# Performance work log

Measured on AMD Instinct MI355X. Metric: run time of the kernel, lower is better.

The kernel has to match this reference:

```python
import jax, jax.numpy as jnp
import numpy as np

# blocks, d_model, heads, ffn_hidden, vocab, gen_len=(image_size//4)**2
L, D, NH, FF, V, GEN = 4, 256, 8, 1024, 2048, 16
B, NS, SLOT = 8, 7, 256  # batch, num_slots+1 (slots + projected action), slot_size


def setup_inputs():
    key = jax.random.key(0)
    ks = jax.random.split(key, 16)
    def n(i, shape, s=0.02):
        return (jax.random.normal(ks[i], shape) * s).astype(jnp.float32)
    return dict(
        slots=jax.random.normal(ks[0], (B, NS, SLOT), dtype=jnp.float32),
        W_slot_proj=n(1, (SLOT, D)),
        dict_emb=n(2, (V + 1, D)),
        pe=n(3, (GEN + 1, D)),
        ln_self_w=jnp.ones((L, D)), ln_self_b=jnp.zeros((L, D)),
        Wq_s=n(4, (L, D, D)), Wk_s=n(5, (L, D, D)), Wv_s=n(6, (L, D, D)), Wo_s=n(7, (L, D, D)),
        ln_cross_w=jnp.ones((L, D)), ln_cross_b=jnp.zeros((L, D)),
        Wq_c=n(8, (L, D, D)), Wk_c=n(9, (L, D, D)), Wv_c=n(10, (L, D, D)), Wo_c=n(11, (L, D, D)),
        ln_ffn_w=jnp.ones((L, D)), ln_ffn_b=jnp.zeros((L, D)),
        W1=n(12, (L, D, FF)), b1=jnp.zeros((L, FF)),
        W2=n(13, (L, FF, D)), b2=jnp.zeros((L, D)),
        ln_f_w=jnp.ones((D,)), ln_f_b=jnp.zeros((D,)),
        W_out=n(14, (D, V)),
    )


def _ln(x, w, b, eps=1e-5):
    m = x.mean(-1, keepdims=True)
    v = ((x - m) ** 2).mean(-1, keepdims=True)
    return (x - m) * jax.lax.rsqrt(v + eps) * w + b


def _mha(q_in, k_in, v_in, Wq, Wk, Wv, Wo, mask=None):
    Bq, Tq, Dm = q_in.shape
    dh = Dm // NH
    q = (q_in @ Wq).reshape(Bq, Tq, NH, dh).transpose(0, 2, 1, 3) * (dh ** -0.5)
    k = (k_in @ Wk).reshape(Bq, -1, NH, dh).transpose(0, 2, 1, 3)
    v = (v_in @ Wv).reshape(Bq, -1, NH, dh).transpose(0, 2, 1, 3)
    att = jnp.einsum('bhqd,bhkd->bhqk', q, k)
    if mask is not None:
        att = att + mask
    att = jax.nn.softmax(att, axis=-1)
    o = jnp.einsum('bhqk,bhkd->bhqd', att, v)
    return o.transpose(0, 2, 1, 3).reshape(Bq, Tq, Dm) @ Wo


def _decoder(x, enc, P):
    T = x.shape[1]
    i = jnp.arange(T)
    mask = jnp.where(i[:, None] >= i[None, :], 0.0, -jnp.inf).astype(x.dtype)
    for l in range(L):
        h = _ln(x, P['ln_self_w'][l], P['ln_self_b'][l])
        if l == 0:
            x = h  # SLATE: first block normalizes residual stream in-place
        x = x + _mha(h, h, h, P['Wq_s'][l], P['Wk_s'][l], P['Wv_s'][l], P['Wo_s'][l], mask)
        h = _ln(x, P['ln_cross_w'][l], P['ln_cross_b'][l])
        x = x + _mha(h, enc, enc, P['Wq_c'][l], P['Wk_c'][l], P['Wv_c'][l], P['Wo_c'][l])
        h = _ln(x, P['ln_ffn_w'][l], P['ln_ffn_b'][l])
        x = x + (jax.nn.relu(h @ P['W1'][l] + P['b1'][l]) @ P['W2'][l] + P['b2'][l])
    return _ln(x, P['ln_f_w'], P['ln_f_b'])


def _slots2tokens(slots, W_slot_proj, dict_emb, pe, P, W_out):
    Bb = slots.shape[0]
    enc = slots @ W_slot_proj  # slot_proj (bias=False)
    Tf = GEN + 1
    # fixed-size token buffer; position 0 is BOS one-hot, future slots are zeros
    # (causal mask guarantees they never influence position t's output)
    buf = jnp.zeros((Bb, Tf, V + 1), jnp.float32).at[:, 0, 0].set(1.0)

    def step(buf, t):
        tok = jnp.argmax(buf, axis=-1)              # [B, Tf]
        emb = dict_emb[tok] + pe[None, :Tf]         # OneHotDictionary + PositionalEncoding
        dec = _decoder(emb, enc, P)
        logits_t = dec[:, t] @ W_out                # [B, V]
        z_next = jax.nn.one_hot(jnp.argmax(logits_t, -1), V, dtype=buf.dtype)
        upd = jnp.pad(z_next, ((0, 0), (1, 0)))[:, None, :]  # prepend BOS column
        buf = jax.lax.dynamic_update_slice(buf, upd, (0, t + 1, 0))
        return buf, (z_next, logits_t)

    _, (z_gen, logits) = jax.lax.scan(step, buf, jnp.arange(GEN))
    z_gen = jnp.moveaxis(z_gen, 0, 1)    # [B, GEN, V]
    logits = jnp.moveaxis(logits, 0, 1)  # [B, GEN, V]
    He = int(np.sqrt(GEN))               # H_enc = W_enc = image_size // 4
    z_img = z_gen.transpose(0, 2, 1).reshape(Bb, V, He, He)
    return z_img, jax.nn.log_softmax(logits, axis=-1)


def reference(slots, W_slot_proj, dict_emb, pe, ln_self_w, ln_self_b, Wq_s, Wk_s, Wv_s, Wo_s, ln_cross_w, ln_cross_b, Wq_c, Wk_c, Wv_c, Wo_c, ln_ffn_w, ln_ffn_b, W1, b1, W2, b2, ln_f_w, ln_f_b, W_out):
    P = dict(ln_self_w=ln_self_w, ln_self_b=ln_self_b, Wq_s=Wq_s, Wk_s=Wk_s, Wv_s=Wv_s, Wo_s=Wo_s,
             ln_cross_w=ln_cross_w, ln_cross_b=ln_cross_b, Wq_c=Wq_c, Wk_c=Wk_c, Wv_c=Wv_c, Wo_c=Wo_c,
             ln_ffn_w=ln_ffn_w, ln_ffn_b=ln_ffn_b, W1=W1, b1=b1, W2=W2, b2=b2,
             ln_f_w=ln_f_w, ln_f_b=ln_f_b)
    return _slots2tokens(slots, W_slot_proj, dict_emb, pe, P, W_out)
```

## Files before the change

### kernel.cpp

```cpp
#include <hip/hip_runtime.h>

#define D       256
#define DH      32
#define FFDIM   1024
#define VOCAB   2048
#define GENLEN  16
#define BATCH   8
#define NSLOT   7
#define TF      17
#define NLAYER  4

#define SCOPE_AGENT __HIP_MEMORY_SCOPE_AGENT

typedef float    f32x4 __attribute__((ext_vector_type(4)));
typedef unsigned u32x4 __attribute__((ext_vector_type(4)));
typedef unsigned long long u64;

struct Params {
  const float *slots, *W_slot_proj, *dict_emb, *pe;
  const float *ln_self_w, *ln_self_b, *Wq_s, *Wk_s, *Wv_s, *Wo_s;
  const float *ln_cross_w, *ln_cross_b, *Wq_c, *Wk_c, *Wv_c, *Wo_c;
  const float *ln_ffn_w, *ln_ffn_b, *W1, *b1, *W2, *b2;
  const float *ln_f_w, *ln_f_b, *W_out;
  float *enc;
  u64 *P0, *P1, *tri;
  unsigned *flags;
  float *out_z, *out_lp;
};

__device__ __forceinline__ float cload(const float* p) {
  return __hip_atomic_load(p, __ATOMIC_RELAXED, SCOPE_AGENT);
}
__device__ __forceinline__ void cstore(float* p, float v) {
  __hip_atomic_store(p, v, __ATOMIC_RELAXED, SCOPE_AGENT);
}
__device__ __forceinline__ u64 cload64(const u64* p) {
  return __hip_atomic_load(p, __ATOMIC_RELAXED, SCOPE_AGENT);
}
__device__ __forceinline__ void cstore64(u64* p, u64 v) {
  __hip_atomic_store(p, v, __ATOMIC_RELAXED, SCOPE_AGENT);
}
__device__ __forceinline__ u64 packt(unsigned tag, float v) {
  return ((u64)tag << 32) | (u64)__float_as_uint(v);
}

__device__ __forceinline__ float blockSum(float v, float* red) {
  #pragma unroll
  for (int o = 32; o > 0; o >>= 1) v += __shfl_down(v, o);
  const int lane = threadIdx.x & 63, w = threadIdx.x >> 6;
  if (lane == 0) red[w] = v;
  __syncthreads();
  float s = red[0] + red[1] + red[2] + red[3];
  __syncthreads();
  return s;
}

template<int N>
__device__ __forceinline__ float dotStreamPre(const float* __restrict__ W,
                                              const float* __restrict__ h,
                                              int i0, int ld,
                                              const float* __restrict__ pre) {
  float pA[32], pB[32];
  #pragma unroll
  for (int k = 0; k < 32; ++k) pA[k] = pre[k];
  #pragma unroll
  for (int k = 0; k < 32; ++k) pB[k] = W[(size_t)(i0 + 32 + k) * ld];
  float acc = 0.f;
  #pragma unroll 1
  for (int u = 0; u < N; u += 64) {
    const f32x4* h4 = reinterpret_cast<const f32x4*>(h + i0 + u);
    #pragma unroll
    for (int k = 0; k < 8; ++k) {
      const f32x4 hv = h4[k];
      acc = fmaf(hv.x, pA[4*k+0], acc); acc = fmaf(hv.y, pA[4*k+1], acc);
      acc = fmaf(hv.z, pA[4*k+2], acc); acc = fmaf(hv.w, pA[4*k+3], acc);
    }
    if (u + 64 < N) {
      #pragma unroll
      for (int k = 0; k < 32; ++k) pA[k] = W[(size_t)(i0 + u + 64 + k) * ld];
    }
    #pragma unroll
    for (int k = 0; k < 8; ++k) {
      const f32x4 hv = h4[8 + k];
      acc = fmaf(hv.x, pB[4*k+0], acc); acc = fmaf(hv.y, pB[4*k+1], acc);
      acc = fmaf(hv.z, pB[4*k+2], acc); acc = fmaf(hv.w, pB[4*k+3], acc);
    }
    if (u + 96 < N) {
      #pragma unroll
      for (int k = 0; k < 32; ++k) pB[k] = W[(size_t)(i0 + u + 96 + k) * ld];
    }
  }
  return acc;
}

template<int N>
__device__ __forceinline__ float dotStream(const float* __restrict__ W,
                                           const float* __restrict__ h,
                                           int i0, int ld) {
  float pre[32];
  #pragma unroll
  for (int k = 0; k < 32; ++k) pre[k] = W[(size_t)(i0 + k) * ld];
  return dotStreamPre<N>(W, h, i0, ld, pre);
}

__device__ __forceinline__ float dot32(const float* __restrict__ w,
                                       const float* __restrict__ h, int i0) {
  float acc = 0.f;
  const f32x4* h4 = reinterpret_cast<const f32x4*>(h + i0);
  #pragma unroll
  for (int k = 0; k < 8; ++k) {
    const f32x4 hv = h4[k];
    acc = fmaf(hv.x, w[4*k+0], acc); acc = fmaf(hv.y, w[4*k+1], acc);
    acc = fmaf(hv.z, w[4*k+2], acc); acc = fmaf(hv.w, w[4*k+3], acc);
  }
  return acc;
}

__global__ __launch_bounds__(256, 1) void mega_kernel(Params p)
{
  const int blk = blockIdx.x;
  const int bb = blk >> 3, sl = blk & 7, tid = threadIdx.x;
  unsigned* flags = p.flags + bb * 256;

  __shared__ __align__(16) float hsh[D];
  __shared__ __align__(16) float ash[128];
  __shared__ float qsh[DH], osh[DH], score[TF], red[4];
  __shared__ float wval[4]; __shared__ int widx[4];
  __shared__ float stage[NSLOT * D];
  __shared__ float kls[NLAYER][TF][DH + 1], vls[NLAYER][TF][DH + 1];
  __shared__ float kcls[NLAYER][NSLOT][DH + 1], vcls[NLAYER][NSLOT][DH + 1];

  auto fold8t = [&](const u64* P, unsigned exp) -> float {
    const u64* a0 = P + (bb * 8 + 0) * 256 + tid;
    const u64* a2 = P + (bb * 8 + 2) * 256 + tid;
    const u64* a4 = P + (bb * 8 + 4) * 256 + tid;
    const u64* a6 = P + (bb * 8 + 6) * 256 + tid;
    u64 v0, v1, v2, v3, v4, v5, v6, v7;
    for (;;) {
      asm volatile(
        "global_load_dwordx2 %0, %8, off sc0 sc1\n\t"
        "global_load_dwordx2 %1, %8, off offset:2048 sc0 sc1\n\t"
        "global_load_dwordx2 %2, %9, off sc0 sc1\n\t"
        "global_load_dwordx2 %3, %9, off offset:2048 sc0 sc1\n\t"
        "global_load_dwordx2 %4, %10, off sc0 sc1\n\t"
        "global_load_dwordx2 %5, %10, off offset:2048 sc0 sc1\n\t"
        "global_load_dwordx2 %6, %11, off sc0 sc1\n\t"
        "global_load_dwordx2 %7, %11, off offset:2048 sc0 sc1\n\t"
        "s_waitcnt vmcnt(0)"
        : "=&v"(v0), "=&v"(v1), "=&v"(v2), "=&v"(v3),
          "=&v"(v4), "=&v"(v5), "=&v"(v6), "=&v"(v7)
        : "v"(a0), "v"(a2), "v"(a4), "v"(a6) : "memory");
      if ((unsigned)(v0 >> 32) == exp && (unsigned)(v1 >> 32) == exp &&
          (unsigned)(v2 >> 32) == exp && (unsigned)(v3 >> 32) == exp &&
          (unsigned)(v4 >> 32) == exp && (unsigned)(v5 >> 32) == exp &&
          (unsigned)(v6 >> 32) == exp && (unsigned)(v7 >> 32) == exp)
        break;
      __builtin_amdgcn_s_sleep(1);
    }
    const float s0 = __uint_as_float((unsigned)v0), s1 = __uint_as_float((unsigned)v1);
    const float s2 = __uint_as_float((unsigned)v2), s3 = __uint_as_float((unsigned)v3);
    const float s4 = __uint_as_float((unsigned)v4), s5 = __uint_as_float((unsigned)v5);
    const float s6 = __uint_as_float((unsigned)v6), s7 = __uint_as_float((unsigned)v7);
    return ((s0 + s1) + (s2 + s3)) + ((s4 + s5) + (s6 + s7));
  };

  float heldLogit = 0.f;
  int   lastAmax  = 0;

  auto consume_tri = [&](int row, unsigned exp) {
    float smax8[8], ssum8[8]; int sarg8[8];
    for (;;) {
      bool ok = true;
      #pragma unroll
      for (int j = 0; j < 8; ++j) {
        const u64 A = cload64(&p.tri[(bb * 8 + j) * 4 + 0]);
        const u64 B = cload64(&p.tri[(bb * 8 + j) * 4 + 1]);
        const u64 C = cload64(&p.tri[(bb * 8 + j) * 4 + 2]);
        ok = ok && ((unsigned)(A >> 32) == exp) && ((unsigned)(B >> 32) == exp)
                && ((unsigned)(C >> 32) == exp);
        smax8[j] = __uint_as_float((unsigned)A);
        ssum8[j] = __uint_as_float((unsigned)B);
        sarg8[j] = (int)(unsigned)C;
      }
      if (ok) break;
      __builtin_amdgcn_s_sleep(1);
    }
    float gm = smax8[0];
    #pragma unroll
    for (int j = 1; j < 8; ++j) gm = fmaxf(gm, smax8[j]);
    float gs = 0.f; float best = -1e30f; int am = 0;
    #pragma unroll
    for (int j = 0; j < 8; ++j) {
      gs += ssum8[j] * expf(smax8[j] - gm);
      if (smax8[j] > best) { best = smax8[j]; am = j * 256 + sarg8[j]; }
    }
    const float lse = gm + logf(gs);
    p.out_lp[(bb * GENLEN + row) * VOCAB + sl * 256 + tid] = heldLogit - lse;
    if (sl == 0 && tid == 0)
      p.out_z[bb * VOCAB * GENLEN + am * GENLEN + row] = 1.0f;
    lastAmax = am;
  };

  for (int i = tid; i < NLAYER * TF * (DH + 1); i += 256) {
    (&kls[0][0][0])[i] = 0.f;
    (&vls[0][0][0])[i] = 0.f;
  }

  if (tid < 32) {
    const int c = sl * 32 + tid;
    float acc[NSLOT] = {0.f,0.f,0.f,0.f,0.f,0.f,0.f};
    #pragma unroll 8
    for (int i = 0; i < D; ++i) {
      const float w = p.W_slot_proj[i * D + c];
      #pragma unroll
      for (int s = 0; s < NSLOT; ++s) acc[s] += p.slots[(bb * NSLOT + s) * D + i] * w;
    }
    for (int s = 0; s < NSLOT; ++s) cstore(&p.enc[(bb * NSLOT + s) * D + c], acc[s]);
  }
  {
    __syncthreads();
    if (tid == 0) __hip_atomic_store(flags + sl, 1u, __ATOMIC_RELAXED, SCOPE_AGENT);
    if (tid == 0) {
      u32x4 f0, f1;
      for (;;) {
        asm volatile(
          "global_load_dwordx4 %0, %2, off sc0 sc1\n\t"
          "global_load_dwordx4 %1, %2, off offset:16 sc0 sc1\n\t"
          "s_waitcnt vmcnt(0)"
          : "=&v"(f0), "=&v"(f1) : "v"(flags) : "memory");
        if (f0.x >= 1u && f0.y >= 1u && f0.z >= 1u && f0.w >= 1u &&
            f1.x >= 1u && f1.y >= 1u && f1.z >= 1u && f1.w >= 1u)
          break;
        __builtin_amdgcn_s_sleep(1);
      }
    }
    __syncthreads();
    asm volatile("" ::: "memory");
  }

  {
    for (int i = tid; i < NSLOT * D; i += 256) stage[i] = cload(&p.enc[bb * NSLOT * D + i]);
    __syncthreads();
    const int l = tid >> 6, g = tid & 63, c32 = g >> 1, mat = g & 1;
    const float* W = (mat ? p.Wv_c : p.Wk_c) + l * D * D + sl * DH + c32;
    float acc[NSLOT] = {0.f,0.f,0.f,0.f,0.f,0.f,0.f};
    #pragma unroll 8
    for (int i = 0; i < D; ++i) {
      const float w = W[i * D];
      #pragma unroll
      for (int s = 0; s < NSLOT; ++s) acc[s] += stage[s * D + i] * w;
    }
    if (mat) { for (int s = 0; s < NSLOT; ++s) vcls[l][s][c32] = acc[s]; }
    else     { for (int s = 0; s < NSLOT; ++s) kcls[l][s][c32] = acc[s]; }
    __syncthreads();
  }

  u64* Pbuf[2] = {p.P0, p.P1};
  int par = 0;
  unsigned ctr = 0;
  float x = 0.f;

  #pragma unroll 1
  for (int t = 0; t < GENLEN; ++t) {
    #pragma unroll 1
    for (int l = 0; l < NLAYER; ++l) {
      {
        const unsigned expect = ctr; ++ctr; const unsigned wtag = ctr;
        const int mm = tid >> 6, g = tid & 63, c32 = g >> 1, half = g & 1;
        const float* Wqkv = (mm == 0 ? p.Wq_s : (mm == 1 ? p.Wk_s : p.Wv_s))
                          + l * D * D + sl * DH + c32;
        float preq[32];
        if (tid < 192) {
          #pragma unroll
          for (int k = 0; k < 32; ++k) preq[k] = Wqkv[(size_t)(half * 128 + k) * D];
        }
        float wo[32];
        {
          const float* W = p.Wo_s + l * D * D + sl * DH * D + tid;
          #pragma unroll
          for (int k = 0; k < 32; ++k) wo[k] = W[(size_t)k * D];
        }

        if (l == 0) {
          int tok = 0;
          if (t > 0) { consume_tri(t - 1, expect); tok = lastAmax + 1; }
          x = p.dict_emb[tok * D + tid] + p.pe[t * D + tid];
        } else {
          x += fold8t(Pbuf[par], expect);
        }
        const float h = blockSum(x, red) * 0.f + x;
        const float mean = blockSum(x, red) * (1.f / D);
        const float dv = x - mean;
        const float var = blockSum(dv * dv, red) * (1.f / D);
        const float hval = dv * (1.f / sqrtf(var + 1e-5f)) * p.ln_self_w[l * D + tid]
                         + p.ln_self_b[l * D + tid];
        (void)h;
        if (l == 0) x = hval;
        hsh[tid] = hval;
        __syncthreads();

        if (tid < 192) {
          float acc = dotStreamPre<128>(Wqkv, hsh, half * 128, D, preq);
          acc += __shfl_xor(acc, 1);
          if (half == 0) {
            if (mm == 0)      qsh[c32] = acc * 0.17677669529663689f;
            else if (mm == 1) kls[l][t][c32] = acc;
            else              vls[l][t][c32] = acc;
          }
        }
        __syncthreads();

        if (tid < 64) {
          float s = -1e30f;
          if (tid <= t) {
            float a = 0.f;
            #pragma unroll
            for (int r = 0; r < DH; ++r) a += qsh[r] * kls[l][tid][r];
            s = a;
          }
          float m = s;
          #pragma unroll
          for (int o = 32; o > 0; o >>= 1) m = fmaxf(m, __shfl_xor(m, o));
          const float e = (tid <= t) ? expf(s - m) : 0.f;
          float sum = e;
          #pragma unroll
          for (int o = 32; o > 0; o >>= 1) sum += __shfl_xor(sum, o);
          const float inv = 1.f / sum;
          if (tid < TF) score[tid] = e * inv;
        }
        __syncthreads();
        if (tid < DH) {
          float a = 0.f;
          #pragma unroll
          for (int pp = 0; pp < TF; ++pp) a = fmaf(score[pp], vls[l][pp][tid], a);
          osh[tid] = a;
        }
        __syncthreads();
        {
          float a0 = 0.f;
          #pragma unroll
          for (int k = 0; k < 32; ++k) a0 = fmaf(osh[k], wo[k], a0);
          cstore64(&Pbuf[par ^ 1][(bb * 8 + sl) * 256 + tid], packt(wtag, a0));
        }
        par ^= 1;
      }

      {
        const unsigned expect = ctr; ++ctr; const unsigned wtag = ctr;
        const int c32 = tid >> 3, sub = tid & 7;
        float wq[32], woc[32];
        {
          const float* W = p.Wq_c + l * D * D + sl * DH + c32;
          #pragma unroll
          for (int k = 0; k < 32; ++k) wq[k] = W[(size_t)(sub * 32 + k) * D];
        }
        {
          const float* W = p.Wo_c + l * D * D + sl * DH * D + tid;
          #pragma unroll
          for (int k = 0; k < 32; ++k) woc[k] = W[(size_t)k * D];
        }

        x += fold8t(Pbuf[par], expect);
        const float mean = blockSum(x, red) * (1.f / D);
        const float dv = x - mean;
        const float var = blockSum(dv * dv, red) * (1.f / D);
        hsh[tid] = dv * (1.f / sqrtf(var + 1e-5f)) * p.ln_cross_w[l * D + tid]
                 + p.ln_cross_b[l * D + tid];
        __syncthreads();

        {
          float acc = dot32(wq, hsh, sub * 32);
          acc += __shfl_xor(acc, 1);
          acc += __shfl_xor(acc, 2);
          acc += __shfl_xor(acc, 4);
          if (sub == 0) qsh[c32] = acc * 0.17677669529663689f;
        }
        __syncthreads();

        if (tid < 64) {
          float s = -1e30f;
          if (tid < NSLOT) {
            float a = 0.f;
            #pragma unroll
            for (int r = 0; r < DH; ++r) a += qsh[r] * kcls[l][tid][r];
            s = a;
          }
          float m = s;
          #pragma unroll
          for (int o = 32; o > 0; o >>= 1) m = fmaxf(m, __shfl_xor(m, o));
          const float e = (tid < NSLOT) ? expf(s - m) : 0.f;
          float sum = e;
          #pragma unroll
          for (int o = 32; o > 0; o >>= 1) sum += __shfl_xor(sum, o);
          const float inv = 1.f / sum;
          if (tid < NSLOT) score[tid] = e * inv;
        }
        __syncthreads();
        if (tid < DH) {
          float a = 0.f;
          #pragma unroll
          for (int s = 0; s < NSLOT; ++s) a = fmaf(score[s], vcls[l][s][tid], a);
          osh[tid] = a;
        }
        __syncthreads();
        {
          float a0 = 0.f;
          #pragma unroll
          for (int k = 0; k < 32; ++k) a0 = fmaf(osh[k], woc[k], a0);
          cstore64(&Pbuf[par ^ 1][(bb * 8 + sl) * 256 + tid], packt(wtag, a0));
        }
        par ^= 1;
      }

      {
        const unsigned expect = ctr; ++ctr; const unsigned wtag = ctr;
        const int c128 = tid >> 1, half = tid & 1, c = sl * 128 + c128;
        const float* W1p = p.W1 + l * D * FFDIM + c;
        float prew1[32];
        {
          #pragma unroll
          for (int k = 0; k < 32; ++k) prew1[k] = W1p[(size_t)(half * 128 + k) * FFDIM];
        }

        x += fold8t(Pbuf[par], expect);
        const float mean = blockSum(x, red) * (1.f / D);
        const float dv = x - mean;
        const float var = blockSum(dv * dv, red) * (1.f / D);
        hsh[tid] = dv * (1.f / sqrtf(var + 1e-5f)) * p.ln_ffn_w[l * D + tid]
                 + p.ln_ffn_b[l * D + tid];
        __syncthreads();

        {
          float acc = dotStreamPre<128>(W1p, hsh, half * 128, FFDIM, prew1);
          acc += __shfl_xor(acc, 1);
          if (half == 0) ash[c128] = fmaxf(acc + p.b1[l * FFDIM + c], 0.f);
        }
        __syncthreads();
        {
          float acc = dotStream<128>(p.W2 + l * FFDIM * D + sl * 128 * D + tid, ash, 0, D);
          if (sl == 0) acc += p.b2[l * D + tid];
          cstore64(&Pbuf[par ^ 1][(bb * 8 + sl) * 256 + tid], packt(wtag, acc));
        }
        __syncthreads();
      }
      par ^= 1;
    }

    {
      const unsigned expect = ctr; ++ctr; const unsigned wtag = ctr;
      const float* Wop = p.W_out + sl * 256 + tid;
      float prewo[32];
      {
        #pragma unroll
        for (int k = 0; k < 32; ++k) prewo[k] = Wop[(size_t)k * VOCAB];
      }

      x += fold8t(Pbuf[par], expect);
      const float mean = blockSum(x, red) * (1.f / D);
      const float dv = x - mean;
      const float var = blockSum(dv * dv, red) * (1.f / D);
      hsh[tid] = dv * (1.f / sqrtf(var + 1e-5f)) * p.ln_f_w[tid] + p.ln_f_b[tid];
      __syncthreads();
      heldLogit = dotStreamPre<256>(Wop, hsh, 0, VOCAB, prewo);

      {
        float v = heldLogit; int idx = tid;
        #pragma unroll
        for (int o = 32; o > 0; o >>= 1) {
          const float v2 = __shfl_xor(v, o);
          const int   i2 = __shfl_xor(idx, o);
          if (v2 > v || (v2 == v && i2 < idx)) { v = v2; idx = i2; }
        }
        const int w = tid >> 6;
        if ((tid & 63) == 0) { wval[w] = v; widx[w] = idx; }
      }
      __syncthreads();
      float smax = wval[0]; int sarg = widx[0];
      #pragma unroll
      for (int j = 1; j < 4; ++j)
        if (wval[j] > smax || (wval[j] == smax && widx[j] < sarg)) { smax = wval[j]; sarg = widx[j]; }
      const float ssum = blockSum(expf(heldLogit - smax), red);
      if (tid == 0) {
        cstore64(&p.tri[(bb * 8 + sl) * 4 + 0], packt(wtag, smax));
        cstore64(&p.tri[(bb * 8 + sl) * 4 + 1], packt(wtag, ssum));
        cstore64(&p.tri[(bb * 8 + sl) * 4 + 2], ((u64)wtag << 32) | (unsigned)sarg);
      }
      __syncthreads();
    }
  }

  consume_tri(GENLEN - 1, ctr);
}

extern "C" void kernel_launch(void* const* d_in, const int* in_sizes, int n_in,
                              void* d_out, int out_size, void* d_ws, size_t ws_size,
                              hipStream_t stream)
{
  Params p;
  const float* const* in = (const float* const*)d_in;
  p.slots = in[0];  p.W_slot_proj = in[1]; p.dict_emb = in[2]; p.pe = in[3];
  p.ln_self_w = in[4];  p.ln_self_b = in[5];
  p.Wq_s = in[6];  p.Wk_s = in[7];  p.Wv_s = in[8];  p.Wo_s = in[9];
  p.ln_cross_w = in[10]; p.ln_cross_b = in[11];
  p.Wq_c = in[12]; p.Wk_c = in[13]; p.Wv_c = in[14]; p.Wo_c = in[15];
  p.ln_ffn_w = in[16]; p.ln_ffn_b = in[17];
  p.W1 = in[18]; p.b1 = in[19]; p.W2 = in[20]; p.b2 = in[21];
  p.ln_f_w = in[22]; p.ln_f_b = in[23]; p.W_out = in[24];

  p.flags = (unsigned*)d_ws;
  p.P0 = (u64*)((char*)d_ws + 8192);
  p.P1 = p.P0 + BATCH * 8 * 256;
  p.tri = p.P1 + BATCH * 8 * 256;
  const size_t zero_bytes = 8192 + 2 * BATCH * 8 * 256 * 8 + BATCH * 8 * 4 * 8;
  p.enc = (float*)((char*)d_ws + ((zero_bytes + 255) & ~(size_t)255));

  p.out_z  = (float*)d_out;
  p.out_lp = (float*)d_out + BATCH * VOCAB * GENLEN;

  hipMemsetAsync(d_ws, 0, zero_bytes, stream);
  hipMemsetAsync(d_out, 0, (size_t)out_size * sizeof(float), stream);

  mega_kernel<<<64, 256, 0, stream>>>(p);
}
```

Baseline: 1.482 ms.

## Split each batch across 16 blocks instead of 8 in persistent megakernel

Doubles the grid from 64 to 128 blocks, so each batch element is handled by 16 cooperating blocks. Each block now owns half a head's output projection, 64 FFN hidden units and 128 vocab columns, which shrinks its serial per-step weight streaming. The cost is a 16-way cross-block partial-sum fold and flag/tri exchange per stage, which means more global polling traffic and synchronisation latency. The W2 weights are also prefetched into registers before the fold, and a dead extra blockSum is removed.

```diff
diff --git a/kernel.cpp b/kernel.cpp
--- a/kernel.cpp
+++ b/kernel.cpp
@@ -9,6 +9,7 @@
 #define NSLOT   7
 #define TF      17
 #define NLAYER  4
+#define NSL     16
 
 #define SCOPE_AGENT __HIP_MEMORY_SCOPE_AGENT
 
@@ -93,14 +94,24 @@
   return acc;
 }
 
-template<int N>
-__device__ __forceinline__ float dotStream(const float* __restrict__ W,
-                                           const float* __restrict__ h,
-                                           int i0, int ld) {
-  float pre[32];
+__device__ __forceinline__ float dot64_2(const float* __restrict__ h, int i0,
+                                         const float* __restrict__ A,
+                                         const float* __restrict__ B) {
+  float acc = 0.f;
+  const f32x4* h4 = reinterpret_cast<const f32x4*>(h + i0);
   #pragma unroll
-  for (int k = 0; k < 32; ++k) pre[k] = W[(size_t)(i0 + k) * ld];
-  return dotStreamPre<N>(W, h, i0, ld, pre);
+  for (int k = 0; k < 8; ++k) {
+    const f32x4 hv = h4[k];
+    acc = fmaf(hv.x, A[4*k+0], acc); acc = fmaf(hv.y, A[4*k+1], acc);
+    acc = fmaf(hv.z, A[4*k+2], acc); acc = fmaf(hv.w, A[4*k+3], acc);
+  }
+  #pragma unroll
+  for (int k = 0; k < 8; ++k) {
+    const f32x4 hv = h4[8 + k];
+    acc = fmaf(hv.x, B[4*k+0], acc); acc = fmaf(hv.y, B[4*k+1], acc);
+    acc = fmaf(hv.z, B[4*k+2], acc); acc = fmaf(hv.w, B[4*k+3], acc);
+  }
+  return acc;
 }
 
 __device__ __forceinline__ float dot32(const float* __restrict__ w,
@@ -119,83 +130,110 @@
 __global__ __launch_bounds__(256, 1) void mega_kernel(Params p)
 {
   const int blk = blockIdx.x;
-  const int bb = blk >> 3, sl = blk & 7, tid = threadIdx.x;
+  const int bb = blk >> 4, sl = blk & 15, tid = threadIdx.x;
+  const int hd = sl >> 1, hf16 = sl & 1;
   unsigned* flags = p.flags + bb * 256;
 
   __shared__ __align__(16) float hsh[D];
-  __shared__ __align__(16) float ash[128];
+  __shared__ __align__(16) float ash[64];
+  __shared__ __align__(16) float lg[128];
   __shared__ float qsh[DH], osh[DH], score[TF], red[4];
-  __shared__ float wval[4]; __shared__ int widx[4];
+  __shared__ float wval[2]; __shared__ int widx[2];
   __shared__ float stage[NSLOT * D];
   __shared__ float kls[NLAYER][TF][DH + 1], vls[NLAYER][TF][DH + 1];
   __shared__ float kcls[NLAYER][NSLOT][DH + 1], vcls[NLAYER][NSLOT][DH + 1];
 
-  auto fold8t = [&](const u64* P, unsigned exp) -> float {
-    const u64* a0 = P + (bb * 8 + 0) * 256 + tid;
-    const u64* a2 = P + (bb * 8 + 2) * 256 + tid;
-    const u64* a4 = P + (bb * 8 + 4) * 256 + tid;
-    const u64* a6 = P + (bb * 8 + 6) * 256 + tid;
-    u64 v0, v1, v2, v3, v4, v5, v6, v7;
+  auto fold16 = [&](const u64* P, unsigned exp) -> float {
+    const u64* b0  = P + (bb * 16 +  0) * 256 + tid;
+    const u64* b2  = P + (bb * 16 +  2) * 256 + tid;
+    const u64* b4  = P + (bb * 16 +  4) * 256 + tid;
+    const u64* b6  = P + (bb * 16 +  6) * 256 + tid;
+    const u64* b8  = P + (bb * 16 +  8) * 256 + tid;
+    const u64* b10 = P + (bb * 16 + 10) * 256 + tid;
+    const u64* b12 = P + (bb * 16 + 12) * 256 + tid;
+    const u64* b14 = P + (bb * 16 + 14) * 256 + tid;
+    u64 v0,v1,v2,v3,v4,v5,v6,v7,v8,v9,v10,v11,v12,v13,v14,v15;
     for (;;) {
       asm volatile(
-        "global_load_dwordx2 %0, %8, off sc0 sc1\n\t"
-        "global_load_dwordx2 %1, %8, off offset:2048 sc0 sc1\n\t"
-        "global_load_dwordx2 %2, %9, off sc0 sc1\n\t"
-        "global_load_dwordx2 %3, %9, off offset:2048 sc0 sc1\n\t"
-        "global_load_dwordx2 %4, %10, off sc0 sc1\n\t"
-        "global_load_dwordx2 %5, %10, off offset:2048 sc0 sc1\n\t"
-        "global_load_dwordx2 %6, %11, off sc0 sc1\n\t"
-        "global_load_dwordx2 %7, %11, off offset:2048 sc0 sc1\n\t"
+        "global_load_dwordx2 %0, %16, off sc0 sc1\n\t"
+        "global_load_dwordx2 %1, %16, off offset:2048 sc0 sc1\n\t"
+        "global_load_dwordx2 %2, %17, off sc0 sc1\n\t"
+        "global_load_dwordx2 %3, %17, off offset:2048 sc0 sc1\n\t"
+        "global_load_dwordx2 %4, %18, off sc0 sc1\n\t"
+        "global_load_dwordx2 %5, %18, off offset:2048 sc0 sc1\n\t"
+        "global_load_dwordx2 %6, %19, off sc0 sc1\n\t"
+        "global_load_dwordx2 %7, %19, off offset:2048 sc0 sc1\n\t"
+        "global_load_dwordx2 %8, %20, off sc0 sc1\n\t"
+        "global_load_dwordx2 %9, %20, off offset:2048 sc0 sc1\n\t"
+        "global_load_dwordx2 %10, %21, off sc0 sc1\n\t"
+        "global_load_dwordx2 %11, %21, off offset:2048 sc0 sc1\n\t"
+        "global_load_dwordx2 %12, %22, off sc0 sc1\n\t"
+        "global_load_dwordx2 %13, %22, off offset:2048 sc0 sc1\n\t"
+        "global_load_dwordx2 %14, %23, off sc0 sc1\n\t"
+        "global_load_dwordx2 %15, %23, off offset:2048 sc0 sc1\n\t"
         "s_waitcnt vmcnt(0)"
         : "=&v"(v0), "=&v"(v1), "=&v"(v2), "=&v"(v3),
-          "=&v"(v4), "=&v"(v5), "=&v"(v6), "=&v"(v7)
-        : "v"(a0), "v"(a2), "v"(a4), "v"(a6) : "memory");
-      if ((unsigned)(v0 >> 32) == exp && (unsigned)(v1 >> 32) == exp &&
-          (unsigned)(v2 >> 32) == exp && (unsigned)(v3 >> 32) == exp &&
-          (unsigned)(v4 >> 32) == exp && (unsigned)(v5 >> 32) == exp &&
-          (unsigned)(v6 >> 32) == exp && (unsigned)(v7 >> 32) == exp)
-        break;
+          "=&v"(v4), "=&v"(v5), "=&v"(v6), "=&v"(v7),
+          "=&v"(v8), "=&v"(v9), "=&v"(v10), "=&v"(v11),
+          "=&v"(v12), "=&v"(v13), "=&v"(v14), "=&v"(v15)
+        : "v"(b0), "v"(b2), "v"(b4), "v"(b6),
+          "v"(b8), "v"(b10), "v"(b12), "v"(b14) : "memory");
+      const unsigned e = exp;
+      bool ok = (unsigned)(v0>>32)==e && (unsigned)(v1>>32)==e &&
+                (unsigned)(v2>>32)==e && (unsigned)(v3>>32)==e &&
+                (unsigned)(v4>>32)==e && (unsigned)(v5>>32)==e &&
+                (unsigned)(v6>>32)==e && (unsigned)(v7>>32)==e &&
+                (unsigned)(v8>>32)==e && (unsigned)(v9>>32)==e &&
+                (unsigned)(v10>>32)==e && (unsigned)(v11>>32)==e &&
+                (unsigned)(v12>>32)==e && (unsigned)(v13>>32)==e &&
+                (unsigned)(v14>>32)==e && (unsigned)(v15>>32)==e;
+      if (ok) break;
       __builtin_amdgcn_s_sleep(1);
     }
-    const float s0 = __uint_as_float((unsigned)v0), s1 = __uint_as_float((unsigned)v1);
-    const float s2 = __uint_as_float((unsigned)v2), s3 = __uint_as_float((unsigned)v3);
-    const float s4 = __uint_as_float((unsigned)v4), s5 = __uint_as_float((unsigned)v5);
-    const float s6 = __uint_as_float((unsigned)v6), s7 = __uint_as_float((unsigned)v7);
-    return ((s0 + s1) + (s2 + s3)) + ((s4 + s5) + (s6 + s7));
+    const float s0=__uint_as_float((unsigned)v0),  s1=__uint_as_float((unsigned)v1);
+    const float s2=__uint_as_float((unsigned)v2),  s3=__uint_as_float((unsigned)v3);
+    const float s4=__uint_as_float((unsigned)v4),  s5=__uint_as_float((unsigned)v5);
+    const float s6=__uint_as_float((unsigned)v6),  s7=__uint_as_float((unsigned)v7);
+    const float s8=__uint_as_float((unsigned)v8),  s9=__uint_as_float((unsigned)v9);
+    const float s10=__uint_as_float((unsigned)v10),s11=__uint_as_float((unsigned)v11);
+    const float s12=__uint_as_float((unsigned)v12),s13=__uint_as_float((unsigned)v13);
+    const float s14=__uint_as_float((unsigned)v14),s15=__uint_as_float((unsigned)v15);
+    return (((s0+s1)+(s2+s3))+((s4+s5)+(s6+s7)))
+         + (((s8+s9)+(s10+s11))+((s12+s13)+(s14+s15)));
   };
 
-  float heldLogit = 0.f;
-  int   lastAmax  = 0;
+  int lastAmax = 0;
 
   auto consume_tri = [&](int row, unsigned exp) {
-    float smax8[8], ssum8[8]; int sarg8[8];
+    float smax16[16], ssum16[16]; int sarg16[16];
     for (;;) {
       bool ok = true;
       #pragma unroll
-      for (int j = 0; j < 8; ++j) {
-        const u64 A = cload64(&p.tri[(bb * 8 + j) * 4 + 0]);
-        const u64 B = cload64(&p.tri[(bb * 8 + j) * 4 + 1]);
-        const u64 C = cload64(&p.tri[(bb * 8 + j) * 4 + 2]);
+      for (int j = 0; j < 16; ++j) {
+        const u64 A = cload64(&p.tri[(bb * 16 + j) * 4 + 0]);
+        const u64 B = cload64(&p.tri[(bb * 16 + j) * 4 + 1]);
+        const u64 C = cload64(&p.tri[(bb * 16 + j) * 4 + 2]);
         ok = ok && ((unsigned)(A >> 32) == exp) && ((unsigned)(B >> 32) == exp)
                 && ((unsigned)(C >> 32) == exp);
-        smax8[j] = __uint_as_float((unsigned)A);
-        ssum8[j] = __uint_as_float((unsigned)B);
-        sarg8[j] = (int)(unsigned)C;
+        smax16[j] = __uint_as_float((unsigned)A);
+        ssum16[j] = __uint_as_float((unsigned)B);
+        sarg16[j] = (int)(unsigned)C;
       }
       if (ok) break;
       __builtin_amdgcn_s_sleep(1);
     }
-    float gm = smax8[0];
+    float gm = smax16[0];
     #pragma unroll
-    for (int j = 1; j < 8; ++j) gm = fmaxf(gm, smax8[j]);
+    for (int j = 1; j < 16; ++j) gm = fmaxf(gm, smax16[j]);
     float gs = 0.f; float best = -1e30f; int am = 0;
     #pragma unroll
-    for (int j = 0; j < 8; ++j) {
-      gs += ssum8[j] * expf(smax8[j] - gm);
-      if (smax8[j] > best) { best = smax8[j]; am = j * 256 + sarg8[j]; }
+    for (int j = 0; j < 16; ++j) {
+      gs += ssum16[j] * expf(smax16[j] - gm);
+      if (smax16[j] > best) { best = smax16[j]; am = j * 128 + sarg16[j]; }
     }
     const float lse = gm + logf(gs);
-    p.out_lp[(bb * GENLEN + row) * VOCAB + sl * 256 + tid] = heldLogit - lse;
+    if (tid < 128)
+      p.out_lp[(bb * GENLEN + row) * VOCAB + sl * 128 + tid] = lg[tid] - lse;
     if (sl == 0 && tid == 0)
       p.out_z[bb * VOCAB * GENLEN + am * GENLEN + row] = 1.0f;
     lastAmax = am;
@@ -206,8 +244,8 @@
     (&vls[0][0][0])[i] = 0.f;
   }
 
-  if (tid < 32) {
-    const int c = sl * 32 + tid;
+  if (tid < 16) {
+    const int c = sl * 16 + tid;
     float acc[NSLOT] = {0.f,0.f,0.f,0.f,0.f,0.f,0.f};
     #pragma unroll 8
     for (int i = 0; i < D; ++i) {
@@ -221,15 +259,17 @@
     __syncthreads();
     if (tid == 0) __hip_atomic_store(flags + sl, 1u, __ATOMIC_RELAXED, SCOPE_AGENT);
     if (tid == 0) {
-      u32x4 f0, f1;
+      u32x4 f0, f1, f2, f3;
       for (;;) {
         asm volatile(
-          "global_load_dwordx4 %0, %2, off sc0 sc1\n\t"
-          "global_load_dwordx4 %1, %2, off offset:16 sc0 sc1\n\t"
+          "global_load_dwordx4 %0, %4, off sc0 sc1\n\t"
+          "global_load_dwordx4 %1, %4, off offset:16 sc0 sc1\n\t"
+          "global_load_dwordx4 %2, %4, off offset:32 sc0 sc1\n\t"
+          "global_load_dwordx4 %3, %4, off offset:48 sc0 sc1\n\t"
           "s_waitcnt vmcnt(0)"
-          : "=&v"(f0), "=&v"(f1) : "v"(flags) : "memory");
-        if (f0.x >= 1u && f0.y >= 1u && f0.z >= 1u && f0.w >= 1u &&
-            f1.x >= 1u && f1.y >= 1u && f1.z >= 1u && f1.w >= 1u)
+          : "=&v"(f0), "=&v"(f1), "=&v"(f2), "=&v"(f3) : "v"(flags) : "memory");
+        if (f0.x && f0.y && f0.z && f0.w && f1.x && f1.y && f1.z && f1.w &&
+            f2.x && f2.y && f2.z && f2.w && f3.x && f3.y && f3.z && f3.w)
           break;
         __builtin_amdgcn_s_sleep(1);
       }
@@ -242,7 +282,7 @@
     for (int i = tid; i < NSLOT * D; i += 256) stage[i] = cload(&p.enc[bb * NSLOT * D + i]);
     __syncthreads();
     const int l = tid >> 6, g = tid & 63, c32 = g >> 1, mat = g & 1;
-    const float* W = (mat ? p.Wv_c : p.Wk_c) + l * D * D + sl * DH + c32;
+    const float* W = (mat ? p.Wv_c : p.Wk_c) + l * D * D + hd * DH + c32;
     float acc[NSLOT] = {0.f,0.f,0.f,0.f,0.f,0.f,0.f};
     #pragma unroll 8
     for (int i = 0; i < D; ++i) {
@@ -268,17 +308,17 @@
         const unsigned expect = ctr; ++ctr; const unsigned wtag = ctr;
         const int mm = tid >> 6, g = tid & 63, c32 = g >> 1, half = g & 1;
         const float* Wqkv = (mm == 0 ? p.Wq_s : (mm == 1 ? p.Wk_s : p.Wv_s))
-                          + l * D * D + sl * DH + c32;
+                          + l * D * D + hd * DH + c32;
         float preq[32];
         if (tid < 192) {
           #pragma unroll
           for (int k = 0; k < 32; ++k) preq[k] = Wqkv[(size_t)(half * 128 + k) * D];
         }
-        float wo[32];
-        {
-          const float* W = p.Wo_s + l * D * D + sl * DH * D + tid;
-          #pragma unroll
-          for (int k = 0; k < 32; ++k) wo[k] = W[(size_t)k * D];
+        float wo[16];
+        {
+          const float* W = p.Wo_s + l * D * D + (hd * DH + hf16 * 16) * D + tid;
+          #pragma unroll
+          for (int k = 0; k < 16; ++k) wo[k] = W[(size_t)k * D];
         }
 
         if (l == 0) {
@@ -286,15 +326,13 @@
           if (t > 0) { consume_tri(t - 1, expect); tok = lastAmax + 1; }
           x = p.dict_emb[tok * D + tid] + p.pe[t * D + tid];
         } else {
-          x += fold8t(Pbuf[par], expect);
-        }
-        const float h = blockSum(x, red) * 0.f + x;
+          x += fold16(Pbuf[par], expect);
+        }
         const float mean = blockSum(x, red) * (1.f / D);
         const float dv = x - mean;
         const float var = blockSum(dv * dv, red) * (1.f / D);
         const float hval = dv * (1.f / sqrtf(var + 1e-5f)) * p.ln_self_w[l * D + tid]
                          + p.ln_self_b[l * D + tid];
-        (void)h;
         if (l == 0) x = hval;
         hsh[tid] = hval;
         __syncthreads();
@@ -339,8 +377,8 @@
         {
           float a0 = 0.f;
           #pragma unroll
-          for (int k = 0; k < 32; ++k) a0 = fmaf(osh[k], wo[k], a0);
-          cstore64(&Pbuf[par ^ 1][(bb * 8 + sl) * 256 + tid], packt(wtag, a0));
+          for (int k = 0; k < 16; ++k) a0 = fmaf(osh[hf16 * 16 + k], wo[k], a0);
+          cstore64(&Pbuf[par ^ 1][(bb * 16 + sl) * 256 + tid], packt(wtag, a0));
         }
         par ^= 1;
       }
@@ -348,19 +386,20 @@
       {
         const unsigned expect = ctr; ++ctr; const unsigned wtag = ctr;
         const int c32 = tid >> 3, sub = tid & 7;
-        float wq[32], woc[32];
-        {
-          const float* W = p.Wq_c + l * D * D + sl * DH + c32;
+        float wq[32];
+        {
+          const float* W = p.Wq_c + l * D * D + hd * DH + c32;
           #pragma unroll
           for (int k = 0; k < 32; ++k) wq[k] = W[(size_t)(sub * 32 + k) * D];
         }
-        {
-          const float* W = p.Wo_c + l * D * D + sl * DH * D + tid;
-          #pragma unroll
-          for (int k = 0; k < 32; ++k) woc[k] = W[(size_t)k * D];
-        }
-
-        x += fold8t(Pbuf[par], expect);
+        float woc[16];
+        {
+          const float* W = p.Wo_c + l * D * D + (hd * DH + hf16 * 16) * D + tid;
+          #pragma unroll
+          for (int k = 0; k < 16; ++k) woc[k] = W[(size_t)k * D];
+        }
+
+        x += fold16(Pbuf[par], expect);
         const float mean = blockSum(x, red) * (1.f / D);
         const float dv = x - mean;
         const float var = blockSum(dv * dv, red) * (1.f / D);
@@ -406,23 +445,31 @@
         {
           float a0 = 0.f;
           #pragma unroll
-          for (int k = 0; k < 32; ++k) a0 = fmaf(osh[k], woc[k], a0);
-          cstore64(&Pbuf[par ^ 1][(bb * 8 + sl) * 256 + tid], packt(wtag, a0));
+          for (int k = 0; k < 16; ++k) a0 = fmaf(osh[hf16 * 16 + k], woc[k], a0);
+          cstore64(&Pbuf[par ^ 1][(bb * 16 + sl) * 256 + tid], packt(wtag, a0));
         }
         par ^= 1;
       }
 
       {
         const unsigned expect = ctr; ++ctr; const unsigned wtag = ctr;
-        const int c128 = tid >> 1, half = tid & 1, c = sl * 128 + c128;
+        const int c64 = tid >> 2, q4 = tid & 3, c = sl * 64 + c64;
         const float* W1p = p.W1 + l * D * FFDIM + c;
-        float prew1[32];
-        {
-          #pragma unroll
-          for (int k = 0; k < 32; ++k) prew1[k] = W1p[(size_t)(half * 128 + k) * FFDIM];
-        }
-
-        x += fold8t(Pbuf[par], expect);
+        float w1A[32], w1B[32];
+        {
+          #pragma unroll
+          for (int k = 0; k < 32; ++k) w1A[k] = W1p[(size_t)(q4 * 64 + k) * FFDIM];
+          #pragma unroll
+          for (int k = 0; k < 32; ++k) w1B[k] = W1p[(size_t)(q4 * 64 + 32 + k) * FFDIM];
+        }
+        const float* W2p = p.W2 + l * FFDIM * D + sl * 64 * D + tid;
+        float prew2[32];
+        {
+          #pragma unroll
+          for (int k = 0; k < 32; ++k) prew2[k] = W2p[(size_t)k * D];
+        }
+
+        x += fold16(Pbuf[par], expect);
         const float mean = blockSum(x, red) * (1.f / D);
         const float dv = x - mean;
         const float var = blockSum(dv * dv, red) * (1.f / D);
@@ -431,15 +478,16 @@
         __syncthreads();
 
         {
-          float acc = dotStreamPre<128>(W1p, hsh, half * 128, FFDIM, prew1);
+          float acc = dot64_2(hsh, q4 * 64, w1A, w1B);
           acc += __shfl_xor(acc, 1);
-          if (half == 0) ash[c128] = fmaxf(acc + p.b1[l * FFDIM + c], 0.f);
-        }
-        __syncthreads();
-        {
-          float acc = dotStream<128>(p.W2 + l * FFDIM * D + sl * 128 * D + tid, ash, 0, D);
+          acc += __shfl_xor(acc, 2);
+          if (q4 == 0) ash[c64] = fmaxf(acc + p.b1[l * FFDIM + c], 0.f);
+        }
+        __syncthreads();
+        {
+          float acc = dotStreamPre<64>(W2p, ash, 0, D, prew2);
           if (sl == 0) acc += p.b2[l * D + tid];
-          cstore64(&Pbuf[par ^ 1][(bb * 8 + sl) * 256 + tid], packt(wtag, acc));
+          cstore64(&Pbuf[par ^ 1][(bb * 16 + sl) * 256 + tid], packt(wtag, acc));
         }
         __syncthreads();
       }
@@ -448,23 +496,30 @@
 
     {
       const unsigned expect = ctr; ++ctr; const unsigned wtag = ctr;
-      const float* Wop = p.W_out + sl * 256 + tid;
+      const int j = tid >> 1, hf = tid & 1;
+      const float* Wop = p.W_out + sl * 128 + j;
       float prewo[32];
       {
         #pragma unroll
-        for (int k = 0; k < 32; ++k) prewo[k] = Wop[(size_t)k * VOCAB];
-      }
-
-      x += fold8t(Pbuf[par], expect);
+        for (int k = 0; k < 32; ++k) prewo[k] = Wop[(size_t)(hf * 128 + k) * VOCAB];
+      }
+
+      x += fold16(Pbuf[par], expect);
       const float mean = blockSum(x, red) * (1.f / D);
       const float dv = x - mean;
       const float var = blockSum(dv * dv, red) * (1.f / D);
       hsh[tid] = dv * (1.f / sqrtf(var + 1e-5f)) * p.ln_f_w[tid] + p.ln_f_b[tid];
       __syncthreads();
-      heldLogit = dotStreamPre<256>(Wop, hsh, 0, VOCAB, prewo);
-
       {
-        float v = heldLogit; int idx = tid;
+        float acc = dotStreamPre<128>(Wop, hsh, hf * 128, VOCAB, prewo);
+        acc += __shfl_xor(acc, 1);
+        if (hf == 0) lg[j] = acc;
+      }
+      __syncthreads();
+
+      float myv = (tid < 128) ? lg[tid] : -1e30f;
+      {
+        float v = myv; int idx = (tid < 128) ? tid : 0x7fffffff;
         #pragma unroll
         for (int o = 32; o > 0; o >>= 1) {
           const float v2 = __shfl_xor(v, o);
@@ -472,18 +527,16 @@
           if (v2 > v || (v2 == v && i2 < idx)) { v = v2; idx = i2; }
         }
         const int w = tid >> 6;
-        if ((tid & 63) == 0) { wval[w] = v; widx[w] = idx; }
+        if (w < 2 && (tid & 63) == 0) { wval[w] = v; widx[w] = idx; }
       }
       __syncthreads();
       float smax = wval[0]; int sarg = widx[0];
-      #pragma unroll
-      for (int j = 1; j < 4; ++j)
-        if (wval[j] > smax || (wval[j] == smax && widx[j] < sarg)) { smax = wval[j]; sarg = widx[j]; }
-      const float ssum = blockSum(expf(heldLogit - smax), red);
+      if (wval[1] > smax || (wval[1] == smax && widx[1] < sarg)) { smax = wval[1]; sarg = widx[1]; }
+      const float ssum = blockSum((tid < 128) ? expf(myv - smax) : 0.f, red);
       if (tid == 0) {
-        cstore64(&p.tri[(bb * 8 + sl) * 4 + 0], packt(wtag, smax));
-        cstore64(&p.tri[(bb * 8 + sl) * 4 + 1], packt(wtag, ssum));
-        cstore64(&p.tri[(bb * 8 + sl) * 4 + 2], ((u64)wtag << 32) | (unsigned)sarg);
+        cstore64(&p.tri[(bb * 16 + sl) * 4 + 0], packt(wtag, smax));
+        cstore64(&p.tri[(bb * 16 + sl) * 4 + 1], packt(wtag, ssum));
+        cstore64(&p.tri[(bb * 16 + sl) * 4 + 2], ((u64)wtag << 32) | (unsigned)sarg);
       }
       __syncthreads();
     }
@@ -509,9 +562,10 @@
 
   p.flags = (unsigned*)d_ws;
   p.P0 = (u64*)((char*)d_ws + 8192);
-  p.P1 = p.P0 + BATCH * 8 * 256;
-  p.tri = p.P1 + BATCH * 8 * 256;
-  const size_t zero_bytes = 8192 + 2 * BATCH * 8 * 256 * 8 + BATCH * 8 * 4 * 8;
+  p.P1 = p.P0 + BATCH * NSL * 256;
+  p.tri = p.P1 + BATCH * NSL * 256;
+  const size_t zero_bytes = 8192 + 2 * (size_t)BATCH * NSL * 256 * 8
+                          + (size_t)BATCH * NSL * 4 * 8;
   p.enc = (float*)((char*)d_ws + ((zero_bytes + 255) & ~(size_t)255));
 
   p.out_z  = (float*)d_out;
@@ -520,5 +574,5 @@
   hipMemsetAsync(d_ws, 0, zero_bytes, stream);
   hipMemsetAsync(d_out, 0, (size_t)out_size * sizeof(float), stream);
 
-  mega_kernel<<<64, 256, 0, stream>>>(p);
-}
+  mega_kernel<<<BATCH * NSL, 256, 0, stream>>>(p);
+}
```

New measurement: 1.342 ms. 9.4% less time.
